# Performance work log

Measured on AMD Instinct MI355X. Metric: run time of the kernel, lower is better.

Reference implementation:

```python
import jax, jax.numpy as jnp
import numpy as np

B, S, D = 2, 2048, 1024
H, DK, DV = 16, 64, 64
DF = 4096
EPS = 1e-5


def _layer_norm(x, g, b):
    mu = jnp.mean(x, axis=-1, keepdims=True)
    var = jnp.mean((x - mu) ** 2, axis=-1, keepdims=True)
    return (x - mu) * jax.lax.rsqrt(var + EPS) * g + b


def setup_inputs() -> dict:
    key = jax.random.key(0)
    ks = jax.random.split(key, 12)
    s = lambda fan_in: 1.0 / np.sqrt(fan_in)
    return {
        "enc_input": jax.random.normal(ks[0], (B, S, D), dtype=jnp.float32),
        "wq": jax.random.uniform(ks[1], (D, H * DK), jnp.float32, -s(D), s(D)),
        "wk": jax.random.uniform(ks[2], (D, H * DK), jnp.float32, -s(D), s(D)),
        "wv": jax.random.uniform(ks[3], (D, H * DV), jnp.float32, -s(D), s(D)),
        "wo": jax.random.uniform(ks[4], (H * DV, D), jnp.float32, -s(H * DV), s(H * DV)),
        "w1": jax.random.uniform(ks[5], (D, DF), jnp.float32, -s(D), s(D)),
        "b1": jax.random.uniform(ks[6], (DF,), jnp.float32, -s(D), s(D)),
        "w2": jax.random.uniform(ks[7], (DF, D), jnp.float32, -s(DF), s(DF)),
        "b2": jax.random.uniform(ks[8], (D,), jnp.float32, -s(DF), s(DF)),
        "ln1_g": jnp.ones((D,), jnp.float32),
        "ln1_b": jnp.zeros((D,), jnp.float32),
        "ln2_g": jnp.ones((D,), jnp.float32),
        "ln2_b": jnp.zeros((D,), jnp.float32),
    }


def reference(enc_input, wq, wk, wv, wo, w1, b1, w2, b2, ln1_g, ln1_b, ln2_g, ln2_b):
    x = enc_input
    # QKV projections -> [B, H, S, d]
    q = (x @ wq).reshape(B, S, H, DK).transpose(0, 2, 1, 3)
    k = (x @ wk).reshape(B, S, H, DK).transpose(0, 2, 1, 3)
    v = (x @ wv).reshape(B, S, H, DV).transpose(0, 2, 1, 3)
    # scaled dot-product attention (scale = 1/sqrt(d_k), dropout is identity at eval)
    score = jnp.einsum("bhqd,bhkd->bhqk", q, k) / jnp.sqrt(jnp.float32(DK))
    attn = jax.nn.softmax(score, axis=-1)
    ctx = jnp.einsum("bhqk,bhkd->bhqd", attn, v)
    ctx = ctx.transpose(0, 2, 1, 3).reshape(B, S, H * DV)
    atn_out = ctx @ wo
    # Add & Norm 1
    h = _layer_norm(x + atn_out, ln1_g, ln1_b)
    # FFN
    ffn = jax.nn.relu(h @ w1 + b1) @ w2 + b2
    # Add & Norm 2
    return _layer_norm(h + ffn, ln2_g, ln2_b)
```

## Files before the change

### kernel.cpp

```cpp
#include <hip/hip_runtime.h>
#include <hip/hip_bf16.h>

typedef __bf16 bf16;
typedef __bf16 bf16x4 __attribute__((ext_vector_type(4)));
typedef __bf16 bf16x8 __attribute__((ext_vector_type(8)));
typedef float  f32x4  __attribute__((ext_vector_type(4)));

#define KB 2
#define KS 2048
#define KD 1024
#define KH 16
#define KM (KB*KS)
#define KQKVN 3072
#define KDF 4096

__device__ __forceinline__ f32x4 mfma16(bf16x8 a, bf16x8 b, f32x4 c) {
  return __builtin_amdgcn_mfma_f32_16x16x32_bf16(a, b, c, 0, 0, 0);
}

__device__ __forceinline__ float exp2_hw(float x) {
  float r;
  asm("v_exp_f32 %0, %1" : "=v"(r) : "v"(x));
  return r;
}

__device__ __forceinline__ void g2l16(const bf16* g, bf16* l) {
  __builtin_amdgcn_global_load_lds(
      (const __attribute__((address_space(1))) unsigned int*)g,
      (__attribute__((address_space(3))) unsigned int*)l, 16, 0, 0);
}

__global__ __launch_bounds__(256) void cvt_bf16_kernel(const float* __restrict__ in,
                                                       bf16* __restrict__ out, int n) {
  int i = (blockIdx.x * 256 + threadIdx.x) * 4;
  if (i >= n) return;
  f32x4 v = *reinterpret_cast<const f32x4*>(in + i);
  bf16x4 o;
  o[0] = (bf16)v[0]; o[1] = (bf16)v[1]; o[2] = (bf16)v[2]; o[3] = (bf16)v[3];
  *reinterpret_cast<bf16x4*>(out + i) = o;
}

struct WT4 { const float* src[4]; bf16* dst[4]; };

__global__ __launch_bounds__(256) void wtrans4_kernel(WT4 jobs) {
  __shared__ float tile[32][33];
  const float* W = jobs.src[blockIdx.z];
  bf16* WT = jobs.dst[blockIdx.z];
  const int n0 = blockIdx.x * 32, k0 = blockIdx.y * 32;
  const int tx = threadIdx.x & 31, ty = threadIdx.x >> 5;
#pragma unroll
  for (int j = ty; j < 32; j += 8) tile[j][tx] = W[(size_t)(k0 + j) * 1024 + n0 + tx];
  __syncthreads();
#pragma unroll
  for (int j = ty; j < 32; j += 8)
    WT[(size_t)(n0 + j) * 1024 + k0 + tx] = (bf16)tile[tx][j];
}

__global__ __launch_bounds__(256) void wtrans_big_kernel(const float* __restrict__ w1,
                                                         bf16* __restrict__ w1T,
                                                         const float* __restrict__ w2,
                                                         bf16* __restrict__ w2T) {
  __shared__ float tile[32][33];
  const float* W; bf16* WT; int K, N, n0, k0;
  if (blockIdx.z == 0) {
    W = w1; WT = w1T; K = 1024; N = 4096;
    n0 = blockIdx.x * 32; k0 = blockIdx.y * 32;
  } else {
    W = w2; WT = w2T; K = 4096; N = 1024;
    n0 = blockIdx.y * 32; k0 = blockIdx.x * 32;
  }
  const int tx = threadIdx.x & 31, ty = threadIdx.x >> 5;
#pragma unroll
  for (int j = ty; j < 32; j += 8) tile[j][tx] = W[(size_t)(k0 + j) * N + n0 + tx];
  __syncthreads();
#pragma unroll
  for (int j = ty; j < 32; j += 8) WT[(size_t)(n0 + j) * K + k0 + tx] = (bf16)tile[tx][j];
}

__global__ __launch_bounds__(256) void kvpack_kernel(const bf16* __restrict__ qkv,
                                                     bf16* __restrict__ kp,
                                                     bf16* __restrict__ vt) {
  __shared__ bf16 tile[64][72];
  const int s0 = blockIdx.x * 64;
  const int bh = blockIdx.y;
  const int b = bh >> 4, h = bh & 15;
  const int t = threadIdx.x;
  const int r = t >> 3, c8 = (t & 7) * 8;
#pragma unroll
  for (int rr = r; rr < 64; rr += 32) {
    const size_t grow = (size_t)(b * KS + s0 + rr) * KQKVN + h * 64 + c8;
    bf16x8 kv = *reinterpret_cast<const bf16x8*>(&qkv[grow + 1024]);
    *reinterpret_cast<bf16x8*>(&kp[((size_t)bh * KS + s0 + rr) * 64 + c8]) = kv;
    bf16x8 vv = *reinterpret_cast<const bf16x8*>(&qkv[grow + 2048]);
#pragma unroll
    for (int j = 0; j < 8; j++) tile[rr][c8 + j] = vv[j];
  }
  __syncthreads();
#pragma unroll
  for (int dd = r; dd < 64; dd += 32) {
    bf16x8 v;
#pragma unroll
    for (int j = 0; j < 8; j++) {
      const int pi = c8 + j;
      const int key = ((pi >> 5) << 5) | (((pi >> 2) & 1) << 4) |
                      (((pi >> 3) & 3) << 2) | (pi & 3);
      v[j] = tile[key][dd];
    }
    *reinterpret_cast<bf16x8*>(&vt[(size_t)bh * 64 * KS + (size_t)dd * KS + s0 + c8]) = v;
  }
}

struct P4 { bf16* p[4]; };

template <typename OUT_T, bool RELU, bool HAS_BIAS, bool SPLITK>
__global__ __launch_bounds__(512, 2) void gemm256(const bf16* __restrict__ A,
                                                  const bf16* __restrict__ BT,
                                                  OUT_T* __restrict__ C, P4 pr,
                                                  const float* __restrict__ bias,
                                                  int M, int N, int K, int Kslice) {
  extern __shared__ __align__(16) bf16 sm[];
  const int tid = threadIdx.x, lane = tid & 63, w = tid >> 6;
  const int wr = w >> 2, wc = w & 3;
  const int gx = gridDim.x;
  const int nwg = gx * gridDim.y;
  int flat = blockIdx.y * gx + blockIdx.x;
  flat = (flat & 7) * (nwg >> 3) + (flat >> 3);
  const int bn = (flat % gx) * 256;
  const int bm = (flat / gx) * 256;
  const int z = blockIdx.z;
  const int NT = (SPLITK ? Kslice : K) >> 5;
  const int lr = lane & 15, hi = lane >> 4;
  int srow[2], scol[2];
#pragma unroll
  for (int j = 0; j < 2; j++) {
    const int u = j * 512 + tid;
    srow[j] = u >> 2;
    scol[j] = (((u & 3) ^ ((u >> 2) & 3))) * 8;
  }
  const bf16* Abase = A + (size_t)bm * K + (SPLITK ? z * Kslice : 0);
  const bf16* Bbase = BT + (size_t)bn * K + (SPLITK ? z * Kslice : 0);
  auto stage = [&](int t) {
    bf16* dst = sm + (size_t)(t & 3) * 16384;
    const int k0 = t * 32;
#pragma unroll
    for (int j = 0; j < 2; j++) {
      g2l16(Abase + (size_t)srow[j] * K + k0 + scol[j], dst + (j * 512 + w * 64) * 8);
      g2l16(Bbase + (size_t)srow[j] * K + k0 + scol[j],
            dst + 8192 + (j * 512 + w * 64) * 8);
    }
  };
  f32x4 acc[8][4] = {};
  stage(0); stage(1); stage(2);
  for (int t = 0; t < NT; t++) {
    const int rem = NT - 1 - t;
    if (rem >= 2)      asm volatile("s_waitcnt vmcnt(8)" ::: "memory");
    else if (rem == 1) asm volatile("s_waitcnt vmcnt(4)" ::: "memory");
    else               asm volatile("s_waitcnt vmcnt(0)" ::: "memory");
    __builtin_amdgcn_sched_barrier(0);
    __builtin_amdgcn_s_barrier();
    __builtin_amdgcn_sched_barrier(0);
    if (t + 3 < NT) stage(t + 3);
    const bf16* sa = sm + (size_t)(t & 3) * 16384;
    const bf16* sb = sa + 8192;
    bf16x8 af[8], bfr[4];
#pragma unroll
    for (int mf = 0; mf < 8; mf++) {
      const int row = wr * 128 + mf * 16 + lr;
      af[mf] = *(const bf16x8*)&sa[row * 32 + ((hi ^ (row & 3)) * 8)];
    }
#pragma unroll
    for (int nf = 0; nf < 4; nf++) {
      const int row = wc * 64 + nf * 16 + lr;
      bfr[nf] = *(const bf16x8*)&sb[row * 32 + ((hi ^ (row & 3)) * 8)];
    }
    __builtin_amdgcn_s_setprio(1);
#pragma unroll
    for (int mf = 0; mf < 8; mf++)
#pragma unroll
      for (int nf = 0; nf < 4; nf++)
        acc[mf][nf] = mfma16(af[mf], bfr[nf], acc[mf][nf]);
    __builtin_amdgcn_s_setprio(0);
  }
  const int rg = hi * 4, cl = lr;
  if (SPLITK) {
    bf16* P = pr.p[z];
#pragma unroll
    for (int mf = 0; mf < 8; mf++)
#pragma unroll
      for (int nf = 0; nf < 4; nf++) {
        const int col = bn + wc * 64 + nf * 16 + cl;
#pragma unroll
        for (int i = 0; i < 4; i++) {
          const int row = bm + wr * 128 + mf * 16 + rg + i;
          P[(size_t)row * N + col] = (bf16)acc[mf][nf][i];
        }
      }
  } else {
#pragma unroll
    for (int mf = 0; mf < 8; mf++)
#pragma unroll
      for (int nf = 0; nf < 4; nf++) {
        const int col = bn + wc * 64 + nf * 16 + cl;
        float bv = 0.f;
        if (HAS_BIAS) bv = bias[col];
#pragma unroll
        for (int i = 0; i < 4; i++) {
          const int row = bm + wr * 128 + mf * 16 + rg + i;
          float v = acc[mf][nf][i] + bv;
          if (RELU) v = fmaxf(v, 0.f);
          C[(size_t)row * N + col] = (OUT_T)v;
        }
      }
  }
}

template <typename OUT_T, bool RELU, bool HAS_BIAS, int BN>
__global__ __launch_bounds__(256) void gemm_bt(const bf16* __restrict__ A,
                                               const bf16* __restrict__ BT,
                                               OUT_T* __restrict__ C,
                                               const float* __restrict__ bias,
                                               int M, int N, int K) {
  constexpr int NF = BN / 32;
  __shared__ __align__(16) bf16 sa[2][128 * 32];
  __shared__ __align__(16) bf16 sb[2][BN * 32];
  const int t = threadIdx.x, lane = t & 63, w = t >> 6;
  const int gx = gridDim.x;
  const int nwg = gx * gridDim.y;
  int flat = blockIdx.y * gx + blockIdx.x;
  if ((nwg & 7) == 0) flat = (flat & 7) * (nwg >> 3) + (flat >> 3);
  const int bn = (flat % gx) * BN;
  const int bm = (flat / gx) * 128;
  const int wr = w >> 1, wc = w & 1;
  const int wcol = wc * (BN / 2);
  const int lr = lane & 15, lk = (lane >> 4) * 8;
  const int srow = w * 16 + (lane >> 2);
  const int scol = (lane & 3) * 8;
  f32x4 acc[4][NF] = {};
  const int NT = K >> 5;
  auto stage = [&](int kt, int buf) {
#pragma unroll
    for (int i = 0; i < 2; i++)
      g2l16(A + (size_t)(bm + i * 64 + srow) * K + kt * 32 + scol,
            &sa[buf][(i * 64 + w * 16) * 32]);
#pragma unroll
    for (int i = 0; i < BN / 64; i++)
      g2l16(BT + (size_t)(bn + i * 64 + srow) * K + kt * 32 + scol,
            &sb[buf][(i * 64 + w * 16) * 32]);
  };
  stage(0, 0);
  int cur = 0;
  for (int kt = 0; kt < NT; kt++) {
    __syncthreads();
    if (kt + 1 < NT) stage(kt + 1, cur ^ 1);
    bf16x8 af[4], bfr[NF];
#pragma unroll
    for (int m = 0; m < 4; m++)
      af[m] = *(const bf16x8*)&sa[cur][(wr * 64 + m * 16 + lr) * 32 + lk];
#pragma unroll
    for (int n = 0; n < NF; n++)
      bfr[n] = *(const bf16x8*)&sb[cur][(wcol + n * 16 + lr) * 32 + lk];
#pragma unroll
    for (int m = 0; m < 4; m++)
#pragma unroll
      for (int n = 0; n < NF; n++)
        acc[m][n] = mfma16(af[m], bfr[n], acc[m][n]);
    cur ^= 1;
  }
  const int rg = (lane >> 4) * 4, cl = lane & 15;
#pragma unroll
  for (int m = 0; m < 4; m++)
#pragma unroll
    for (int n = 0; n < NF; n++) {
      const int col = bn + wcol + n * 16 + cl;
      float bv = 0.f;
      if (HAS_BIAS) bv = bias[col];
#pragma unroll
      for (int i = 0; i < 4; i++) {
        const int row = bm + wr * 64 + m * 16 + rg + i;
        float v = acc[m][n][i] + bv;
        if (RELU) v = fmaxf(v, 0.f);
        C[(size_t)row * N + col] = (OUT_T)v;
      }
    }
}

__global__ __launch_bounds__(256) void attn_kernel(const bf16* __restrict__ qkv,
                                                   const bf16* __restrict__ kp,
                                                   const bf16* __restrict__ vt,
                                                   bf16* __restrict__ ctx) {
  __shared__ __align__(16) bf16 ksm[4][64 * 64];
  __shared__ __align__(16) bf16 vsm[4][64 * 64];
  const int t = threadIdx.x, lane = t & 63, w = t >> 6;
  const int flat = blockIdx.y * 16 + blockIdx.x;
  const int xcd = flat & 7, jj = flat >> 3;
  const int bh = xcd + 8 * (jj >> 4);
  const int qb = jj & 15;
  const int b = bh >> 4, h = bh & 15;
  const int qbase = qb * 128 + w * 32;
  const int lr = lane & 15, hi = lane >> 4;
  const int lk = hi * 8, rg = hi * 4, cl = lr;

  bf16x8 aq[2][2];
#pragma unroll
  for (int m = 0; m < 2; m++)
#pragma unroll
    for (int kk = 0; kk < 2; kk++) {
      bf16x8 v = *reinterpret_cast<const bf16x8*>(
          &qkv[(size_t)(b * KS + qbase + m * 16 + lr) * KQKVN + h * 64 + kk * 32 + lk]);
#pragma unroll
      for (int e = 0; e < 8; e++) v[e] = (bf16)((float)v[e] * 0.18033688f);
      aq[m][kk] = v;
    }
  bf16x8 ones;
#pragma unroll
  for (int j = 0; j < 8; j++) ones[j] = (bf16)1.0f;

  const bf16* kpb = kp + (size_t)bh * KS * 64;
  const bf16* vtb = vt + (size_t)bh * 64 * KS;

  auto stageKV = [&](int tt) {
    const int kt0 = tt * 64;
    bf16* kd = &ksm[tt & 3][0];
    bf16* vd = &vsm[tt & 3][0];
#pragma unroll
    for (int i = 0; i < 2; i++) {
      const int q = i * 4096 + w * 1024 + (lane << 4);
      const int row = q >> 7;
      const int slot = ((q >> 4) & 7) ^ (row & 7);
      g2l16(kpb + (size_t)(kt0 + row) * 64 + slot * 8, kd + ((i * 4096 + w * 1024) >> 1));
      g2l16(vtb + (size_t)row * KS + kt0 + slot * 8,   vd + ((i * 4096 + w * 1024) >> 1));
    }
  };

  f32x4 accd[2][4] = {};
  f32x4 lsumv[2] = {};

  stageKV(0); stageKV(1); stageKV(2);
  const int NT = KS / 64;
  for (int tt = 0; tt < NT; tt++) {
    const int rem = NT - 1 - tt;
    if (rem >= 2)      asm volatile("s_waitcnt vmcnt(8)" ::: "memory");
    else if (rem == 1) asm volatile("s_waitcnt vmcnt(4)" ::: "memory");
    else               asm volatile("s_waitcnt vmcnt(0)" ::: "memory");
    __builtin_amdgcn_sched_barrier(0);
    __builtin_amdgcn_s_barrier();
    __builtin_amdgcn_sched_barrier(0);
    if (tt + 3 < NT) stageKV(tt + 3);
    const char* kb = (const char*)&ksm[tt & 3][0];
    const char* vb = (const char*)&vsm[tt & 3][0];
    bf16x8 bk[4][2];
#pragma unroll
    for (int n = 0; n < 4; n++)
#pragma unroll
      for (int kk = 0; kk < 2; kk++) {
        const int row = n * 16 + lr;
        bk[n][kk] = *(const bf16x8*)(kb + row * 128 +
                                     ((kk * 64 + hi * 16) ^ ((row & 7) << 4)));
      }
    f32x4 sc[2][4] = {};
    __builtin_amdgcn_s_setprio(1);
#pragma unroll
    for (int m = 0; m < 2; m++)
#pragma unroll
      for (int n = 0; n < 4; n++)
#pragma unroll
        for (int kk = 0; kk < 2; kk++)
          sc[m][n] = mfma16(bk[n][kk], aq[m][kk], sc[m][n]);
    __builtin_amdgcn_s_setprio(0);
    bf16x8 pa[2][2];
#pragma unroll
    for (int m = 0; m < 2; m++) {
      float p[4][4];
#pragma unroll
      for (int n = 0; n < 4; n++)
#pragma unroll
        for (int i = 0; i < 4; i++)
          p[n][i] = exp2_hw(sc[m][n][i]);
#pragma unroll
      for (int kk = 0; kk < 2; kk++) {
        bf16x8 v;
#pragma unroll
        for (int j = 0; j < 8; j++) v[j] = (bf16)p[kk * 2 + (j >> 2)][j & 3];
        pa[m][kk] = v;
      }
    }
    bf16x8 bv[4][2];
#pragma unroll
    for (int dt = 0; dt < 4; dt++)
#pragma unroll
      for (int kk = 0; kk < 2; kk++) {
        const int row = dt * 16 + lr;
        bv[dt][kk] = *(const bf16x8*)(vb + row * 128 +
                                      ((kk * 64 + hi * 16) ^ ((row & 7) << 4)));
      }
    __builtin_amdgcn_s_setprio(1);
#pragma unroll
    for (int m = 0; m < 2; m++) {
#pragma unroll
      for (int dt = 0; dt < 4; dt++)
#pragma unroll
        for (int kk = 0; kk < 2; kk++)
          accd[m][dt] = mfma16(pa[m][kk], bv[dt][kk], accd[m][dt]);
      lsumv[m] = mfma16(pa[m][0], ones, lsumv[m]);
      lsumv[m] = mfma16(pa[m][1], ones, lsumv[m]);
    }
    __builtin_amdgcn_s_setprio(0);
  }
#pragma unroll
  for (int m = 0; m < 2; m++)
#pragma unroll
    for (int dt = 0; dt < 4; dt++)
#pragma unroll
      for (int i = 0; i < 4; i++)
        ctx[(size_t)(b * KS + qbase + m * 16 + rg + i) * KD + h * 64 + dt * 16 + cl] =
            (bf16)(accd[m][dt][i] / lsumv[m][i]);
}

template <bool ABF, bool OBF>
__global__ __launch_bounds__(256) void ln_kernel(const void* __restrict__ aptr,
                                                 const float* __restrict__ bsum,
                                                 const float* __restrict__ g,
                                                 const float* __restrict__ bet,
                                                 void* __restrict__ outp) {
  const int row = blockIdx.x;
  const int t = threadIdx.x;
  const int lane = t & 63, wid = t >> 6;
  float v[4];
  {
    f32x4 bv = *reinterpret_cast<const f32x4*>(&bsum[(size_t)row * KD + t * 4]);
    if (ABF) {
      bf16x4 av = *reinterpret_cast<const bf16x4*>(
          (const bf16*)aptr + (size_t)row * KD + t * 4);
#pragma unroll
      for (int j = 0; j < 4; j++) v[j] = (float)av[j] + bv[j];
    } else {
      f32x4 av = *reinterpret_cast<const f32x4*>(
          (const float*)aptr + (size_t)row * KD + t * 4);
#pragma unroll
      for (int j = 0; j < 4; j++) v[j] = av[j] + bv[j];
    }
  }
  float s = 0.f, s2 = 0.f;
#pragma unroll
  for (int j = 0; j < 4; j++) { s += v[j]; s2 += v[j] * v[j]; }
#pragma unroll
  for (int off = 32; off; off >>= 1) {
    s += __shfl_xor(s, off, 64);
    s2 += __shfl_xor(s2, off, 64);
  }
  __shared__ float red[8];
  if (lane == 0) { red[wid] = s; red[wid + 4] = s2; }
  __syncthreads();
  s = red[0] + red[1] + red[2] + red[3];
  s2 = red[4] + red[5] + red[6] + red[7];
  const float mu = s * (1.f / KD);
  const float var = s2 * (1.f / KD) - mu * mu;
  const float rs = rsqrtf(var + 1e-5f);
  if (OBF) {
    bf16x4 o;
#pragma unroll
    for (int j = 0; j < 4; j++)
      o[j] = (bf16)((v[j] - mu) * rs * g[t * 4 + j] + bet[t * 4 + j]);
    *reinterpret_cast<bf16x4*>((bf16*)outp + (size_t)row * KD + t * 4) = o;
  } else {
    f32x4 o;
#pragma unroll
    for (int j = 0; j < 4; j++)
      o[j] = (v[j] - mu) * rs * g[t * 4 + j] + bet[t * 4 + j];
    *reinterpret_cast<f32x4*>((float*)outp + (size_t)row * KD + t * 4) = o;
  }
}

__global__ __launch_bounds__(256) void ln2_fused_kernel(const bf16* __restrict__ hh,
                                                        const bf16* __restrict__ p0,
                                                        const bf16* __restrict__ p1,
                                                        const bf16* __restrict__ p2,
                                                        const bf16* __restrict__ p3,
                                                        const float* __restrict__ b2,
                                                        const float* __restrict__ g,
                                                        const float* __restrict__ bet,
                                                        float* __restrict__ outp) {
  const int row = blockIdx.x;
  const int t = threadIdx.x;
  const int lane = t & 63, wid = t >> 6;
  const size_t base = (size_t)row * KD + t * 4;
  bf16x4 hv = *(const bf16x4*)(hh + base);
  bf16x4 a0 = *(const bf16x4*)(p0 + base);
  bf16x4 a1 = *(const bf16x4*)(p1 + base);
  bf16x4 a2 = *(const bf16x4*)(p2 + base);
  bf16x4 a3 = *(const bf16x4*)(p3 + base);
  f32x4 bv = *(const f32x4*)(b2 + t * 4);
  float v[4];
#pragma unroll
  for (int j = 0; j < 4; j++)
    v[j] = (float)hv[j] + (float)a0[j] + (float)a1[j] + (float)a2[j] + (float)a3[j] + bv[j];
  float s = 0.f, s2 = 0.f;
#pragma unroll
  for (int j = 0; j < 4; j++) { s += v[j]; s2 += v[j] * v[j]; }
#pragma unroll
  for (int off = 32; off; off >>= 1) {
    s += __shfl_xor(s, off, 64);
    s2 += __shfl_xor(s2, off, 64);
  }
  __shared__ float red[8];
  if (lane == 0) { red[wid] = s; red[wid + 4] = s2; }
  __syncthreads();
  s = red[0] + red[1] + red[2] + red[3];
  s2 = red[4] + red[5] + red[6] + red[7];
  const float mu = s * (1.f / KD);
  const float var = s2 * (1.f / KD) - mu * mu;
  const float rs = rsqrtf(var + 1e-5f);
  f32x4 o;
#pragma unroll
  for (int j = 0; j < 4; j++)
    o[j] = (v[j] - mu) * rs * g[t * 4 + j] + bet[t * 4 + j];
  *reinterpret_cast<f32x4*>(outp + base) = o;
}

extern "C" void kernel_launch(void* const* d_in, const int* in_sizes, int n_in,
                              void* d_out, int out_size, void* d_ws, size_t ws_size,
                              hipStream_t stream) {
  const float* x     = (const float*)d_in[0];
  const float* wq    = (const float*)d_in[1];
  const float* wk    = (const float*)d_in[2];
  const float* wv    = (const float*)d_in[3];
  const float* wo    = (const float*)d_in[4];
  const float* w1    = (const float*)d_in[5];
  const float* b1    = (const float*)d_in[6];
  const float* w2    = (const float*)d_in[7];
  const float* b2    = (const float*)d_in[8];
  const float* ln1g  = (const float*)d_in[9];
  const float* ln1b  = (const float*)d_in[10];
  const float* ln2g  = (const float*)d_in[11];
  const float* ln2b  = (const float*)d_in[12];
  float* out = (float*)d_out;

  char* ws = (char*)d_ws;
  bf16*  x_bf   = (bf16*)(ws + 0);
  bf16*  wqkvT  = (bf16*)(ws + 8388608);
  bf16*  woT    = (bf16*)(ws + 14680064);
  bf16*  w1T    = (bf16*)(ws + 16777216);
  bf16*  w2T    = (bf16*)(ws + 25165824);
  bf16*  qkv    = (bf16*)(ws + 33554432);
  bf16*  kp     = (bf16*)(ws + 58720256);
  bf16*  vt     = (bf16*)(ws + 67108864);
  float* proj   = (float*)(ws + 75497472);
  bf16*  ctx    = x_bf;
  bf16*  h_bf   = (bf16*)(ws + 8388608);
  bf16*  ffn1   = qkv;
  P4 pr;
  pr.p[0] = (bf16*)(ws + 0);
  pr.p[1] = (bf16*)(ws + 16777216);
  pr.p[2] = (bf16*)(ws + 67108864);
  pr.p[3] = (bf16*)(ws + 75497472);
  P4 pzero = {};

  cvt_bf16_kernel<<<dim3(KM * KD / 1024), 256, 0, stream>>>(x, x_bf, KM * KD);
  WT4 jobs;
  jobs.src[0] = wq; jobs.src[1] = wk; jobs.src[2] = wv; jobs.src[3] = wo;
  jobs.dst[0] = wqkvT;
  jobs.dst[1] = wqkvT + 1024 * 1024;
  jobs.dst[2] = wqkvT + 2048 * 1024;
  jobs.dst[3] = woT;
  wtrans4_kernel<<<dim3(32, 32, 4), 256, 0, stream>>>(jobs);
  wtrans_big_kernel<<<dim3(128, 32, 2), 256, 0, stream>>>(w1, w1T, w2, w2T);

  gemm256<bf16, false, false, false>
      <<<dim3(KQKVN / 256, KM / 256, 1), 512, 131072, stream>>>(
      x_bf, wqkvT, qkv, pzero, nullptr, KM, KQKVN, KD, KD);

  kvpack_kernel<<<dim3(KS / 64, KB * KH), 256, 0, stream>>>(qkv, kp, vt);

  attn_kernel<<<dim3(KS / 128, KB * KH), 256, 0, stream>>>(qkv, kp, vt, ctx);

  gemm_bt<float, false, false, 64><<<dim3(KD / 64, KM / 128), 256, 0, stream>>>(
      ctx, woT, proj, nullptr, KM, KD, KD);

  ln_kernel<false, true><<<dim3(KM), 256, 0, stream>>>(x, proj, ln1g, ln1b, h_bf);

  gemm256<bf16, true, true, false>
      <<<dim3(KDF / 256, KM / 256, 1), 512, 131072, stream>>>(
      h_bf, w1T, ffn1, pzero, b1, KM, KDF, KD, KD);

  gemm256<bf16, false, false, true>
      <<<dim3(KD / 256, KM / 256, 4), 512, 131072, stream>>>(
      ffn1, w2T, (bf16*)nullptr, pr, nullptr, KM, KD, KDF, KDF / 4);

  ln2_fused_kernel<<<dim3(KM), 256, 0, stream>>>(
      h_bf, pr.p[0], pr.p[1], pr.p[2], pr.p[3], b2, ln2g, ln2b, out);
}
```

Baseline: 228.4 us.

## Restructure 256x256 GEMM into 8-phase ping-pong pipeline with K=64 tiles

```diff
diff --git a/kernel.cpp b/kernel.cpp
--- a/kernel.cpp
+++ b/kernel.cpp
@@ -113,11 +113,11 @@
 struct P4 { bf16* p[4]; };
 
 template <typename OUT_T, bool RELU, bool HAS_BIAS, bool SPLITK>
-__global__ __launch_bounds__(512, 2) void gemm256(const bf16* __restrict__ A,
-                                                  const bf16* __restrict__ BT,
-                                                  OUT_T* __restrict__ C, P4 pr,
-                                                  const float* __restrict__ bias,
-                                                  int M, int N, int K, int Kslice) {
+__global__ __launch_bounds__(512, 2) void gemm8p(const bf16* __restrict__ A,
+                                                 const bf16* __restrict__ BT,
+                                                 OUT_T* __restrict__ C, P4 pr,
+                                                 const float* __restrict__ bias,
+                                                 int M, int N, int K, int Kslice) {
   extern __shared__ __align__(16) bf16 sm[];
   const int tid = threadIdx.x, lane = tid & 63, w = tid >> 6;
   const int wr = w >> 2, wc = w & 3;
@@ -128,58 +128,115 @@
   const int bn = (flat % gx) * 256;
   const int bm = (flat / gx) * 256;
   const int z = blockIdx.z;
-  const int NT = (SPLITK ? Kslice : K) >> 5;
+  const int NT = (SPLITK ? Kslice : K) >> 6;
   const int lr = lane & 15, hi = lane >> 4;
-  int srow[2], scol[2];
-#pragma unroll
-  for (int j = 0; j < 2; j++) {
-    const int u = j * 512 + tid;
-    srow[j] = u >> 2;
-    scol[j] = (((u & 3) ^ ((u >> 2) & 3))) * 8;
-  }
+  const int sqrow = tid >> 3;
+  const int sslot = tid & 7;
   const bf16* Abase = A + (size_t)bm * K + (SPLITK ? z * Kslice : 0);
   const bf16* Bbase = BT + (size_t)bn * K + (SPLITK ? z * Kslice : 0);
-  auto stage = [&](int t) {
-    bf16* dst = sm + (size_t)(t & 3) * 16384;
-    const int k0 = t * 32;
-#pragma unroll
-    for (int j = 0; j < 2; j++) {
-      g2l16(Abase + (size_t)srow[j] * K + k0 + scol[j], dst + (j * 512 + w * 64) * 8);
-      g2l16(Bbase + (size_t)srow[j] * K + k0 + scol[j],
-            dst + 8192 + (j * 512 + w * 64) * 8);
-    }
+  auto stageQ = [&](int t, int p) {
+    const int row = p * 64 + sqrow;
+    const int col = (sslot ^ (row & 7)) * 8;
+    bf16* dst = sm + (size_t)(t & 1) * 32768 + p * 4096 + w * 512;
+    g2l16(Abase + (size_t)row * K + t * 64 + col, dst);
+    g2l16(Bbase + (size_t)row * K + t * 64 + col, dst + 16384);
   };
   f32x4 acc[8][4] = {};
-  stage(0); stage(1); stage(2);
+  stageQ(0, 0); stageQ(0, 1); stageQ(0, 2); stageQ(0, 3);
   for (int t = 0; t < NT; t++) {
-    const int rem = NT - 1 - t;
-    if (rem >= 2)      asm volatile("s_waitcnt vmcnt(8)" ::: "memory");
-    else if (rem == 1) asm volatile("s_waitcnt vmcnt(4)" ::: "memory");
-    else               asm volatile("s_waitcnt vmcnt(0)" ::: "memory");
+    const char* sa = (const char*)(sm + (size_t)(t & 1) * 32768);
+    const char* sb = sa + 32768;
+    bf16x8 af[4], bfr[4];
+    if (t + 1 < NT) {
+      stageQ(t + 1, 0);
+      asm volatile("s_waitcnt vmcnt(2)" ::: "memory");
+    } else {
+      asm volatile("s_waitcnt vmcnt(0)" ::: "memory");
+    }
     __builtin_amdgcn_sched_barrier(0);
     __builtin_amdgcn_s_barrier();
     __builtin_amdgcn_sched_barrier(0);
-    if (t + 3 < NT) stage(t + 3);
-    const bf16* sa = sm + (size_t)(t & 3) * 16384;
-    const bf16* sb = sa + 8192;
-    bf16x8 af[8], bfr[4];
-#pragma unroll
-    for (int mf = 0; mf < 8; mf++) {
-      const int row = wr * 128 + mf * 16 + lr;
-      af[mf] = *(const bf16x8*)&sa[row * 32 + ((hi ^ (row & 3)) * 8)];
+#pragma unroll
+    for (int mfp = 0; mfp < 4; mfp++) {
+      const int row = wr * 128 + mfp * 16 + lr;
+      af[mfp] = *(const bf16x8*)(sa + row * 128 + ((hi ^ (row & 7)) * 16));
     }
 #pragma unroll
     for (int nf = 0; nf < 4; nf++) {
       const int row = wc * 64 + nf * 16 + lr;
-      bfr[nf] = *(const bf16x8*)&sb[row * 32 + ((hi ^ (row & 3)) * 8)];
-    }
+      bfr[nf] = *(const bf16x8*)(sb + row * 128 + ((hi ^ (row & 7)) * 16));
+    }
+    asm volatile("s_waitcnt lgkmcnt(0)" ::: "memory");
+    __builtin_amdgcn_sched_barrier(0);
     __builtin_amdgcn_s_setprio(1);
 #pragma unroll
-    for (int mf = 0; mf < 8; mf++)
+    for (int mfp = 0; mfp < 4; mfp++)
 #pragma unroll
       for (int nf = 0; nf < 4; nf++)
-        acc[mf][nf] = mfma16(af[mf], bfr[nf], acc[mf][nf]);
+        acc[mfp][nf] = mfma16(af[mfp], bfr[nf], acc[mfp][nf]);
     __builtin_amdgcn_s_setprio(0);
+    if (t + 1 < NT) stageQ(t + 1, 1);
+#pragma unroll
+    for (int mfp = 0; mfp < 4; mfp++) {
+      const int row = wr * 128 + 64 + mfp * 16 + lr;
+      af[mfp] = *(const bf16x8*)(sa + row * 128 + ((hi ^ (row & 7)) * 16));
+    }
+    __builtin_amdgcn_sched_barrier(0);
+    __builtin_amdgcn_s_barrier();
+    __builtin_amdgcn_sched_barrier(0);
+    asm volatile("s_waitcnt lgkmcnt(0)" ::: "memory");
+    __builtin_amdgcn_sched_barrier(0);
+    __builtin_amdgcn_s_setprio(1);
+#pragma unroll
+    for (int mfp = 0; mfp < 4; mfp++)
+#pragma unroll
+      for (int nf = 0; nf < 4; nf++)
+        acc[4 + mfp][nf] = mfma16(af[mfp], bfr[nf], acc[4 + mfp][nf]);
+    __builtin_amdgcn_s_setprio(0);
+    if (t + 1 < NT) stageQ(t + 1, 2);
+#pragma unroll
+    for (int mfp = 0; mfp < 4; mfp++) {
+      const int row = wr * 128 + mfp * 16 + lr;
+      af[mfp] = *(const bf16x8*)(sa + row * 128 + (((4 + hi) ^ (row & 7)) * 16));
+    }
+#pragma unroll
+    for (int nf = 0; nf < 4; nf++) {
+      const int row = wc * 64 + nf * 16 + lr;
+      bfr[nf] = *(const bf16x8*)(sb + row * 128 + (((4 + hi) ^ (row & 7)) * 16));
+    }
+    __builtin_amdgcn_sched_barrier(0);
+    __builtin_amdgcn_s_barrier();
+    __builtin_amdgcn_sched_barrier(0);
+    asm volatile("s_waitcnt lgkmcnt(0)" ::: "memory");
+    __builtin_amdgcn_sched_barrier(0);
+    __builtin_amdgcn_s_setprio(1);
+#pragma unroll
+    for (int mfp = 0; mfp < 4; mfp++)
+#pragma unroll
+      for (int nf = 0; nf < 4; nf++)
+        acc[mfp][nf] = mfma16(af[mfp], bfr[nf], acc[mfp][nf]);
+    __builtin_amdgcn_s_setprio(0);
+    if (t + 1 < NT) stageQ(t + 1, 3);
+#pragma unroll
+    for (int mfp = 0; mfp < 4; mfp++) {
+      const int row = wr * 128 + 64 + mfp * 16 + lr;
+      af[mfp] = *(const bf16x8*)(sa + row * 128 + (((4 + hi) ^ (row & 7)) * 16));
+    }
+    __builtin_amdgcn_sched_barrier(0);
+    __builtin_amdgcn_s_barrier();
+    __builtin_amdgcn_sched_barrier(0);
+    asm volatile("s_waitcnt lgkmcnt(0)" ::: "memory");
+    __builtin_amdgcn_sched_barrier(0);
+    __builtin_amdgcn_s_setprio(1);
+#pragma unroll
+    for (int mfp = 0; mfp < 4; mfp++)
+#pragma unroll
+      for (int nf = 0; nf < 4; nf++)
+        acc[4 + mfp][nf] = mfma16(af[mfp], bfr[nf], acc[4 + mfp][nf]);
+    __builtin_amdgcn_s_setprio(0);
+    __builtin_amdgcn_sched_barrier(0);
+    __builtin_amdgcn_s_barrier();
+    __builtin_amdgcn_sched_barrier(0);
   }
   const int rg = hi * 4, cl = lr;
   if (SPLITK) {
@@ -565,7 +622,7 @@
   wtrans4_kernel<<<dim3(32, 32, 4), 256, 0, stream>>>(jobs);
   wtrans_big_kernel<<<dim3(128, 32, 2), 256, 0, stream>>>(w1, w1T, w2, w2T);
 
-  gemm256<bf16, false, false, false>
+  gemm8p<bf16, false, false, false>
       <<<dim3(KQKVN / 256, KM / 256, 1), 512, 131072, stream>>>(
       x_bf, wqkvT, qkv, pzero, nullptr, KM, KQKVN, KD, KD);
 
@@ -578,11 +635,11 @@
 
   ln_kernel<false, true><<<dim3(KM), 256, 0, stream>>>(x, proj, ln1g, ln1b, h_bf);
 
-  gemm256<bf16, true, true, false>
+  gemm8p<bf16, true, true, false>
       <<<dim3(KDF / 256, KM / 256, 1), 512, 131072, stream>>>(
       h_bf, w1T, ffn1, pzero, b1, KM, KDF, KD, KD);
 
-  gemm256<bf16, false, false, true>
+  gemm8p<bf16, false, false, true>
       <<<dim3(KD / 256, KM / 256, 4), 512, 131072, stream>>>(
       ffn1, w2T, (bf16*)nullptr, pr, nullptr, KM, KD, KDF, KDF / 4);
 
```

Measured after the change: 224.2 us. About the same (-1.8%).
